# Performance work log

Measured on AMD Instinct MI355X. Metric: run time of the kernel, lower is better.

## Reference

```python
import jax, jax.numpy as jnp
import numpy as np


def setup_inputs() -> dict:
    key = jax.random.key(0)
    k1, k2 = jax.random.split(key)
    B, N, M = 8, 4096, 4096
    points1 = jax.random.normal(k1, (B, N, 3), dtype=jnp.float32)
    points2 = jax.random.normal(k2, (B, M, 3), dtype=jnp.float32)
    return {"points1": points1, "points2": points2}


def reference(points1, points2):
    x2 = jnp.sum(points1 * points1, axis=-1)            # [B, N]
    y2 = jnp.sum(points2 * points2, axis=-1)            # [B, M]
    xy = jnp.einsum('bnd,bmd->bnm', points1, points2)   # [B, N, M]
    d = x2[:, :, None] + y2[:, None, :] - 2.0 * xy      # [B, N, M]
    dist1 = jnp.min(d, axis=2)                          # [B, N] NN dist p1->p2
    dist2 = jnp.min(d, axis=1)                          # [B, M] NN dist p2->p1
    # Symmetric Hausdorff: max over each direction, then max of the two, sum over batch
    m = jnp.maximum(jnp.max(dist1, axis=-1), jnp.max(dist2, axis=-1))  # [B]
    return jnp.sum(m)
```

## Files before the change

### kernel.cpp

```cpp
#include <hip/hip_runtime.h>
#include <float.h>

#define B_CONST 8
#define GROUPS 16
#define QSPLIT 8

typedef float v2f __attribute__((ext_vector_type(2)));

__global__ void hd_pack(const float* __restrict__ p1, const float* __restrict__ p2,
                        float4* __restrict__ o1, float4* __restrict__ o2,
                        unsigned int* __restrict__ comm, int n1, int n2) {
    int i = blockIdx.x * blockDim.x + threadIdx.x;
    if (blockIdx.x == 0 && threadIdx.x < 9) comm[threadIdx.x] = 0u;
    const float* src; float4* dst; int idx;
    if (i < n1)           { src = p1; dst = o1; idx = i; }
    else if (i < n1 + n2) { src = p2; dst = o2; idx = i - n1; }
    else return;
    size_t s = 3 * (size_t)idx;
    float x = src[s], y = src[s + 1], z = src[s + 2];
    dst[idx] = make_float4(x, y, z, fmaf(x, x, fmaf(y, y, z * z)));
}

__global__ __launch_bounds__(256) void hd_nnmax(
    const float4* __restrict__ qpt1, const float4* __restrict__ qpt2,
    float* __restrict__ part, int N, int M, int blocksDir0) {
    int blk = blockIdx.x;
    const float4* q; const float4* r; int QN, RM, dir;
    if (blk < blocksDir0) { q = qpt1; r = qpt2; QN = N; RM = M; dir = 0; }
    else { blk -= blocksDir0; q = qpt2; r = qpt1; QN = M; RM = N; dir = 1; }

    int qblocks = QN >> 10;
    int perB = qblocks * GROUPS;
    int b    = blk / perB;
    int rem  = blk - b * perB;
    int qblk = rem / GROUPS;
    int g    = rem - qblk * GROUPS;

    int l = threadIdx.x & 63;
    int w = __builtin_amdgcn_readfirstlane((int)(threadIdx.x >> 6));

    __shared__ float red[4096];
    __shared__ float qw_s[1024];

    const float4* qb = q + (size_t)b * QN + ((size_t)qblk << 10);
    v2f NX[8], NY[8], NZ[8], MN[8];
    #pragma unroll
    for (int p = 0; p < 8; ++p) {
        float4 q0 = qb[(2 * p) * 64 + l];
        float4 q1 = qb[(2 * p + 1) * 64 + l];
        NX[p] = (v2f){ -2.0f * q0.x, -2.0f * q1.x };
        NY[p] = (v2f){ -2.0f * q0.y, -2.0f * q1.y };
        NZ[p] = (v2f){ -2.0f * q0.z, -2.0f * q1.z };
        MN[p] = (v2f){ FLT_MAX, FLT_MAX };
        if (w == 0) {
            qw_s[(2 * p) * 64 + l]     = q0.w;
            qw_s[(2 * p + 1) * 64 + l] = q1.w;
        }
    }

    int cnt = RM >> 6;
    const float4* rb = r + (size_t)b * RM + (size_t)(g * 4 + w) * cnt;

    #pragma unroll 4
    for (int j = 0; j < cnt; ++j) {
        float4 rf = rb[j];
        v2f rx = (v2f){ rf.x, rf.x };
        v2f ry = (v2f){ rf.y, rf.y };
        v2f rz = (v2f){ rf.z, rf.z };
        v2f rw = (v2f){ rf.w, rf.w };
        #pragma unroll
        for (int p = 0; p < 8; ++p) {
            v2f a = __builtin_elementwise_fma(NX[p], rx, rw);
            a = __builtin_elementwise_fma(NY[p], ry, a);
            a = __builtin_elementwise_fma(NZ[p], rz, a);
            MN[p] = __builtin_elementwise_min(MN[p], a);
        }
    }

    #pragma unroll
    for (int p = 0; p < 8; ++p) {
        red[(w << 10) + (2 * p) * 64 + l]     = MN[p].x;
        red[(w << 10) + (2 * p + 1) * 64 + l] = MN[p].y;
    }
    __syncthreads();

    size_t dirOff = dir ? (size_t)GROUPS * B_CONST * N : 0;
    float* pb = part + dirOff + ((size_t)g * B_CONST + b) * QN + ((size_t)qblk << 10);
    for (int t = threadIdx.x; t < 1024; t += 256) {
        float m = fminf(fminf(red[t], red[1024 + t]),
                        fminf(red[2048 + t], red[3072 + t]));
        pb[t] = fmaxf(qw_s[t] + m, 0.0f);
    }
}

__global__ __launch_bounds__(256) void hd_final(
    const float* __restrict__ part, unsigned int* __restrict__ comm,
    float* __restrict__ out, int N, int M) {
    int db  = blockIdx.x >> 3;
    int qs  = blockIdx.x & (QSPLIT - 1);
    int dir = db >> 3;
    int b   = db & 7;
    int QN  = dir ? M : N;
    size_t dirOff = dir ? (size_t)GROUPS * B_CONST * N : 0;
    const float* fb = part + dirOff + (size_t)b * QN;
    size_t gs = (size_t)B_CONST * QN;

    int span = QN / QSPLIT;
    int q0 = qs * span;
    float mx = 0.0f;
    for (int qq = q0 + threadIdx.x; qq < q0 + span; qq += 256) {
        float mm = fb[qq];
        #pragma unroll
        for (int gg = 1; gg < GROUPS; ++gg)
            mm = fminf(mm, fb[(size_t)gg * gs + qq]);
        mx = fmaxf(mx, mm);
    }
    #pragma unroll
    for (int off = 32; off > 0; off >>= 1)
        mx = fmaxf(mx, __shfl_down(mx, off, 64));
    __shared__ float wred[4];
    int l = threadIdx.x & 63, w = threadIdx.x >> 6;
    if (l == 0) wred[w] = mx;
    __syncthreads();
    if (threadIdx.x == 0) {
        mx = fmaxf(fmaxf(wred[0], wred[1]), fmaxf(wred[2], wred[3]));
        atomicMax(&comm[b], __float_as_uint(mx));
        __threadfence();
        unsigned int t2 = atomicAdd(&comm[8], 1u);
        if (t2 == (unsigned int)(16 * QSPLIT - 1)) {
            float s = 0.0f;
            for (int bb = 0; bb < B_CONST; ++bb)
                s += __uint_as_float(atomicMax(&comm[bb], 0u));
            out[0] = s;
        }
    }
}

extern "C" void kernel_launch(void* const* d_in, const int* in_sizes, int n_in,
                              void* d_out, int out_size, void* d_ws, size_t ws_size,
                              hipStream_t stream) {
    const float* p1 = (const float*)d_in[0];
    const float* p2 = (const float*)d_in[1];
    const int B = B_CONST;
    int N = in_sizes[0] / (3 * B);
    int M = in_sizes[1] / (3 * B);
    int n1 = B * N, n2 = B * M;

    char* ws = (char*)d_ws;
    float4* qpt1 = (float4*)ws;
    float4* qpt2 = (float4*)(ws + (size_t)n1 * sizeof(float4));
    float* part  = (float*)(ws + (size_t)(n1 + n2) * sizeof(float4));
    unsigned int* comm = (unsigned int*)(part + (size_t)GROUPS * (n1 + n2));

    int packBlocks = (n1 + n2 + 255) / 256;
    hd_pack<<<packBlocks, 256, 0, stream>>>(p1, p2, qpt1, qpt2, comm, n1, n2);

    int blocksDir0 = B * (N >> 10) * GROUPS;
    int blocksDir1 = B * (M >> 10) * GROUPS;
    hd_nnmax<<<blocksDir0 + blocksDir1, 256, 0, stream>>>(
        qpt1, qpt2, part, N, M, blocksDir0);

    hd_final<<<16 * QSPLIT, 256, 0, stream>>>(part, comm, (float*)d_out, N, M);
}
```

Measured before the change: 85.23 us.

## Pack reference points as paired SoA v2f and vectorize across reference pairs

The pack kernel now writes reference points in a paired structure-of-arrays layout with -2x, -2y, -2z and |p|^2 interleaved for two points. The inner loop loads v2f pairs of reference points directly instead of broadcasting one float4 into both lanes. Each thread now holds 8 query points instead of 16, so there are twice as many blocks and each reference load is reused across fewer queries. Query coordinates are read from the raw arrays and |q|^2 is recomputed in the epilogue. The aim is to remove the per-iteration broadcast moves so the packed FMAs work on distinct reference points, at the cost of more reference loads per FMA.

```diff
diff --git a/kernel.cpp b/kernel.cpp
--- a/kernel.cpp
+++ b/kernel.cpp
@@ -8,28 +8,31 @@
 typedef float v2f __attribute__((ext_vector_type(2)));
 
 __global__ void hd_pack(const float* __restrict__ p1, const float* __restrict__ p2,
-                        float4* __restrict__ o1, float4* __restrict__ o2,
+                        float* __restrict__ o1, float* __restrict__ o2,
                         unsigned int* __restrict__ comm, int n1, int n2) {
     int i = blockIdx.x * blockDim.x + threadIdx.x;
     if (blockIdx.x == 0 && threadIdx.x < 9) comm[threadIdx.x] = 0u;
-    const float* src; float4* dst; int idx;
+    const float* src; float* dst; int idx;
     if (i < n1)           { src = p1; dst = o1; idx = i; }
     else if (i < n1 + n2) { src = p2; dst = o2; idx = i - n1; }
     else return;
     size_t s = 3 * (size_t)idx;
     float x = src[s], y = src[s + 1], z = src[s + 2];
-    dst[idx] = make_float4(x, y, z, fmaf(x, x, fmaf(y, y, z * z)));
+    float w = fmaf(x, x, fmaf(y, y, z * z));
+    float* base = dst + (size_t)(idx >> 1) * 8 + (idx & 1);
+    base[0] = -2.0f * x; base[2] = -2.0f * y; base[4] = -2.0f * z; base[6] = w;
 }
 
 __global__ __launch_bounds__(256) void hd_nnmax(
-    const float4* __restrict__ qpt1, const float4* __restrict__ qpt2,
+    const float* __restrict__ p1raw, const float* __restrict__ p2raw,
+    const float* __restrict__ pk1, const float* __restrict__ pk2,
     float* __restrict__ part, int N, int M, int blocksDir0) {
     int blk = blockIdx.x;
-    const float4* q; const float4* r; int QN, RM, dir;
-    if (blk < blocksDir0) { q = qpt1; r = qpt2; QN = N; RM = M; dir = 0; }
-    else { blk -= blocksDir0; q = qpt2; r = qpt1; QN = M; RM = N; dir = 1; }
+    const float* qraw; const float* rpk; int QN, RM, dir;
+    if (blk < blocksDir0) { qraw = p1raw; rpk = pk2; QN = N; RM = M; dir = 0; }
+    else { blk -= blocksDir0; qraw = p2raw; rpk = pk1; QN = M; RM = N; dir = 1; }
 
-    int qblocks = QN >> 10;
+    int qblocks = QN >> 9;
     int perB = qblocks * GROUPS;
     int b    = blk / perB;
     int rem  = blk - b * perB;
@@ -39,57 +42,51 @@
     int l = threadIdx.x & 63;
     int w = __builtin_amdgcn_readfirstlane((int)(threadIdx.x >> 6));
 
-    __shared__ float red[4096];
-    __shared__ float qw_s[1024];
+    const float* qb = qraw + 3 * ((size_t)b * QN + ((size_t)qblk << 9));
+    v2f QX[8], QY[8], QZ[8], MN[8];
+    #pragma unroll
+    for (int s = 0; s < 8; ++s) {
+        int q = s * 64 + l;
+        float x = qb[3 * q], y = qb[3 * q + 1], z = qb[3 * q + 2];
+        QX[s] = (v2f){ x, x };
+        QY[s] = (v2f){ y, y };
+        QZ[s] = (v2f){ z, z };
+        MN[s] = (v2f){ FLT_MAX, FLT_MAX };
+    }
 
-    const float4* qb = q + (size_t)b * QN + ((size_t)qblk << 10);
-    v2f NX[8], NY[8], NZ[8], MN[8];
-    #pragma unroll
-    for (int p = 0; p < 8; ++p) {
-        float4 q0 = qb[(2 * p) * 64 + l];
-        float4 q1 = qb[(2 * p + 1) * 64 + l];
-        NX[p] = (v2f){ -2.0f * q0.x, -2.0f * q1.x };
-        NY[p] = (v2f){ -2.0f * q0.y, -2.0f * q1.y };
-        NZ[p] = (v2f){ -2.0f * q0.z, -2.0f * q1.z };
-        MN[p] = (v2f){ FLT_MAX, FLT_MAX };
-        if (w == 0) {
-            qw_s[(2 * p) * 64 + l]     = q0.w;
-            qw_s[(2 * p + 1) * 64 + l] = q1.w;
+    int cnt = RM / (2 * GROUPS * 4);
+    const v2f* rb = (const v2f*)rpk +
+        ((size_t)b * (RM >> 1) + (size_t)(g * 4 + w) * cnt) * 4;
+
+    #pragma unroll 4
+    for (int j = 0; j < cnt; ++j) {
+        v2f RX = rb[4 * j + 0];
+        v2f RY = rb[4 * j + 1];
+        v2f RZ = rb[4 * j + 2];
+        v2f RW = rb[4 * j + 3];
+        #pragma unroll
+        for (int s = 0; s < 8; ++s) {
+            v2f a = __builtin_elementwise_fma(QX[s], RX, RW);
+            a = __builtin_elementwise_fma(QY[s], RY, a);
+            a = __builtin_elementwise_fma(QZ[s], RZ, a);
+            MN[s] = __builtin_elementwise_min(MN[s], a);
         }
     }
 
-    int cnt = RM >> 6;
-    const float4* rb = r + (size_t)b * RM + (size_t)(g * 4 + w) * cnt;
-
-    #pragma unroll 4
-    for (int j = 0; j < cnt; ++j) {
-        float4 rf = rb[j];
-        v2f rx = (v2f){ rf.x, rf.x };
-        v2f ry = (v2f){ rf.y, rf.y };
-        v2f rz = (v2f){ rf.z, rf.z };
-        v2f rw = (v2f){ rf.w, rf.w };
-        #pragma unroll
-        for (int p = 0; p < 8; ++p) {
-            v2f a = __builtin_elementwise_fma(NX[p], rx, rw);
-            a = __builtin_elementwise_fma(NY[p], ry, a);
-            a = __builtin_elementwise_fma(NZ[p], rz, a);
-            MN[p] = __builtin_elementwise_min(MN[p], a);
-        }
-    }
-
+    __shared__ float red[2048];
     #pragma unroll
-    for (int p = 0; p < 8; ++p) {
-        red[(w << 10) + (2 * p) * 64 + l]     = MN[p].x;
-        red[(w << 10) + (2 * p + 1) * 64 + l] = MN[p].y;
-    }
+    for (int s = 0; s < 8; ++s)
+        red[(w << 9) + s * 64 + l] = fminf(MN[s].x, MN[s].y);
     __syncthreads();
 
     size_t dirOff = dir ? (size_t)GROUPS * B_CONST * N : 0;
-    float* pb = part + dirOff + ((size_t)g * B_CONST + b) * QN + ((size_t)qblk << 10);
-    for (int t = threadIdx.x; t < 1024; t += 256) {
-        float m = fminf(fminf(red[t], red[1024 + t]),
-                        fminf(red[2048 + t], red[3072 + t]));
-        pb[t] = fmaxf(qw_s[t] + m, 0.0f);
+    float* pb = part + dirOff + ((size_t)g * B_CONST + b) * QN + ((size_t)qblk << 9);
+    for (int t = threadIdx.x; t < 512; t += 256) {
+        float m = fminf(fminf(red[t], red[512 + t]),
+                        fminf(red[1024 + t], red[1536 + t]));
+        float x = qb[3 * t], y = qb[3 * t + 1], z = qb[3 * t + 2];
+        float w2 = fmaf(x, x, fmaf(y, y, z * z));
+        pb[t] = fmaxf(w2 + m, 0.0f);
     }
 }
 
@@ -147,18 +144,18 @@
     int n1 = B * N, n2 = B * M;
 
     char* ws = (char*)d_ws;
-    float4* qpt1 = (float4*)ws;
-    float4* qpt2 = (float4*)(ws + (size_t)n1 * sizeof(float4));
-    float* part  = (float*)(ws + (size_t)(n1 + n2) * sizeof(float4));
+    float* pk1 = (float*)ws;
+    float* pk2 = (float*)(ws + (size_t)n1 * 4 * sizeof(float));
+    float* part = (float*)(ws + (size_t)(n1 + n2) * 4 * sizeof(float));
     unsigned int* comm = (unsigned int*)(part + (size_t)GROUPS * (n1 + n2));
 
     int packBlocks = (n1 + n2 + 255) / 256;
-    hd_pack<<<packBlocks, 256, 0, stream>>>(p1, p2, qpt1, qpt2, comm, n1, n2);
+    hd_pack<<<packBlocks, 256, 0, stream>>>(p1, p2, pk1, pk2, comm, n1, n2);
 
-    int blocksDir0 = B * (N >> 10) * GROUPS;
-    int blocksDir1 = B * (M >> 10) * GROUPS;
+    int blocksDir0 = B * (N >> 9) * GROUPS;
+    int blocksDir1 = B * (M >> 9) * GROUPS;
     hd_nnmax<<<blocksDir0 + blocksDir1, 256, 0, stream>>>(
-        qpt1, qpt2, part, N, M, blocksDir0);
+        p1, p2, pk1, pk2, part, N, M, blocksDir0);
 
     hd_final<<<16 * QSPLIT, 256, 0, stream>>>(part, comm, (float*)d_out, N, M);
 }
```

New measurement: 83.39 us. -2.2%, faster.
